# Kernel tuning notes

Measured on AMD Instinct MI355X. Metric: run time of the kernel, lower is better.

## Reference

```python
import jax, jax.numpy as jnp
import numpy as np

NUM_HEADS = 16

def setup_inputs() -> dict:
    key = jax.random.key(0)
    ks = jax.random.split(key, 5)
    b, s, d = 4, 1024, 1024
    scale = 0.02
    return {
        "x": jax.random.normal(ks[0], (b, s, d), dtype=jnp.float32),
        "Wq": jax.random.normal(ks[1], (d, d), dtype=jnp.float32) * scale,
        "Wk": jax.random.normal(ks[2], (d, d), dtype=jnp.float32) * scale,
        "Wv": jax.random.normal(ks[3], (d, d), dtype=jnp.float32) * scale,
        "Wo": jax.random.normal(ks[4], (d, d), dtype=jnp.float32) * scale,
        "bo": jnp.zeros((d,), dtype=jnp.float32),
    }

def reference(x, Wq, Wk, Wv, Wo, bo):
    b, s, d_in = x.shape
    h = NUM_HEADS
    hd = Wq.shape[0] // h  # head_dim
    # torch Linear: y = x @ W.T ; reshape to [b, s, h, hd] then transpose to [b, h, s, hd]
    q = (x @ Wq.T).reshape(b, s, h, hd).transpose(0, 2, 1, 3)
    k = (x @ Wk.T).reshape(b, s, h, hd).transpose(0, 2, 1, 3)
    v = (x @ Wv.T).reshape(b, s, h, hd).transpose(0, 2, 1, 3)
    # attention scores [b, h, s, s]
    scores = jnp.einsum('bhqd,bhkd->bhqk', q, k)
    # NOTE: the original calls masked_fill (NOT masked_fill_), which returns a
    # new tensor that is discarded -> the causal mask is never actually applied.
    # We faithfully reproduce that: no mask.
    attn = jax.nn.softmax(scores / jnp.sqrt(jnp.float32(hd)), axis=-1)
    # dropout p=0.0 -> identity
    ctx = jnp.einsum('bhqk,bhkd->bhqd', attn, v)  # [b, h, s, hd]
    ctx = ctx.transpose(0, 2, 1, 3).reshape(b, s, h * hd)
    return ctx @ Wo.T + bo
```

## Files before the change

kernel.cpp:

```cpp
#include <hip/hip_runtime.h>
#include <hip/hip_bf16.h>

#define BB 4
#define SS 1024
#define DD 1024
#define HH 16
#define HDIM 64
#define MM (BB*SS)

typedef __attribute__((ext_vector_type(8))) short  bf16x8;
typedef __attribute__((ext_vector_type(4))) float  f32x4v;
typedef __attribute__((ext_vector_type(4))) unsigned short u16x4;

static __device__ __forceinline__ unsigned short f2bf(float f) {
    union { float f; unsigned u; } v; v.f = f;
    unsigned r = v.u + 0x7fff + ((v.u >> 16) & 1);
    return (unsigned short)(r >> 16);
}

static __device__ __forceinline__ void gload16(const void* g, const void* lds_uniform_base) {
    __builtin_amdgcn_global_load_lds(
        (const __attribute__((address_space(1))) unsigned int*)(uintptr_t)g,
        (__attribute__((address_space(3))) unsigned int*)(uintptr_t)lds_uniform_base,
        16, 0, 0);
}

__global__ __launch_bounds__(256) void convert_x(
    const float* __restrict__ x, unsigned short* __restrict__ xb)
{
    size_t i = ((size_t)blockIdx.x * 256 + threadIdx.x) * 4;
    f32x4v v = *(const f32x4v*)(x + i);
    u16x4 o;
    o[0] = f2bf(v[0]); o[1] = f2bf(v[1]); o[2] = f2bf(v[2]); o[3] = f2bf(v[3]);
    *(u16x4*)(xb + i) = o;
}

__global__ __launch_bounds__(256) void qkv_gemm(
    const unsigned short* __restrict__ xb,
    const float* __restrict__ Wq, const float* __restrict__ Wk,
    const float* __restrict__ Wv,
    unsigned short* __restrict__ q_ws, unsigned short* __restrict__ k_ws,
    unsigned short* __restrict__ v_ws)
{
    const int bn = blockIdx.x, bm = blockIdx.y, bz = blockIdx.z;
    const float* W = (bz == 0) ? Wq : (bz == 1) ? Wk : Wv;
    unsigned short* outp = (bz == 0) ? q_ws : (bz == 1) ? k_ws : v_ws;

    const int tid = threadIdx.x;
    const int wid = tid >> 6, lane = tid & 63;
    const int wr = wid >> 1, wc = wid & 1;
    const int lhi = lane >> 4, llo = lane & 15;

    __shared__ unsigned short As[2][128 * 32];
    __shared__ unsigned short Bs[2][128 * 32];

    const int m0 = bm * 128, n0 = bn * 128;
    const int brow = tid >> 1, bhalf = tid & 1;

    auto stageA = [&](int buf, int kt) {
        #pragma unroll
        for (int j = 0; j < 2; ++j) {
            int chunk = j * 256 + wid * 64 + lane;
            int row = chunk >> 2, sub = chunk & 3;
            gload16(xb + (size_t)(m0 + row) * DD + kt * 32 + sub * 8,
                    &As[buf][(j * 256 + wid * 64) * 8]);
        }
    };
    auto loadB = [&](int kt, f32x4v* r) {
        const float* p = W + (size_t)(n0 + brow) * DD + kt * 32 + bhalf * 16;
        r[0] = *(const f32x4v*)(p);
        r[1] = *(const f32x4v*)(p + 4);
        r[2] = *(const f32x4v*)(p + 8);
        r[3] = *(const f32x4v*)(p + 12);
    };
    auto writeB = [&](int buf, const f32x4v* r) {
        bf16x8 p0, p1;
        #pragma unroll
        for (int e = 0; e < 4; ++e) {
            p0[e]     = (short)f2bf(r[0][e]);
            p0[e + 4] = (short)f2bf(r[1][e]);
            p1[e]     = (short)f2bf(r[2][e]);
            p1[e + 4] = (short)f2bf(r[3][e]);
        }
        *(bf16x8*)&Bs[buf][brow * 32 + bhalf * 16]     = p0;
        *(bf16x8*)&Bs[buf][brow * 32 + bhalf * 16 + 8] = p1;
    };

    f32x4v acc[4][4] = {};
    f32x4v br[4];

    stageA(0, 0);
    loadB(0, br);
    writeB(0, br);
    __syncthreads();

    for (int kt = 0; kt < 32; ++kt) {
        int cur = kt & 1;
        if (kt < 31) { loadB(kt + 1, br); stageA(cur ^ 1, kt + 1); }

        bf16x8 af[4], bfr[4];
        #pragma unroll
        for (int i = 0; i < 4; ++i)
            af[i] = *(const bf16x8*)&As[cur][(wr * 64 + i * 16 + llo) * 32 + lhi * 8];
        #pragma unroll
        for (int i = 0; i < 4; ++i)
            bfr[i] = *(const bf16x8*)&Bs[cur][(wc * 64 + i * 16 + llo) * 32 + lhi * 8];

        #pragma unroll
        for (int i = 0; i < 4; ++i)
            #pragma unroll
            for (int j = 0; j < 4; ++j)
                acc[i][j] = __builtin_amdgcn_mfma_f32_16x16x32_bf16(af[i], bfr[j], acc[i][j], 0, 0, 0);

        if (kt < 31) writeB(cur ^ 1, br);
        __syncthreads();
    }

    const float sc = (bz == 0) ? 0.125f : 1.0f;
    #pragma unroll
    for (int i = 0; i < 4; ++i) {
        #pragma unroll
        for (int j = 0; j < 4; ++j) {
            #pragma unroll
            for (int r = 0; r < 4; ++r) {
                int mrow = m0 + wr * 64 + i * 16 + lhi * 4 + r;
                int ncol = n0 + wc * 64 + j * 16 + llo;
                float val = acc[i][j][r] * sc;
                size_t idx = ((size_t)((mrow >> 10) * HH + (ncol >> 6)) * SS + (mrow & 1023)) * HDIM + (ncol & 63);
                outp[idx] = f2bf(val);
            }
        }
    }
}

__global__ __launch_bounds__(256) void attn_kernel(
    const unsigned short* __restrict__ q_ws,
    const unsigned short* __restrict__ k_ws,
    const unsigned short* __restrict__ v_ws,
    unsigned short* __restrict__ ctx)
{
    const int qt = blockIdx.x;
    const int bh = blockIdx.y;
    const int tid = threadIdx.x, wid = tid >> 6, lane = tid & 63;
    const int lhi = lane >> 4, llo = lane & 15;

    __shared__ unsigned short Ks[2][64 * 64];
    __shared__ unsigned short Vs[2][64 * 64];
    __shared__ unsigned short Ps[4][16 * 72];

    const size_t basekv = (size_t)bh * SS * HDIM;
    const int qrow0 = qt * 64 + wid * 16;

    bf16x8 aq[2];
    #pragma unroll
    for (int ks = 0; ks < 2; ++ks)
        aq[ks] = *(const bf16x8*)(q_ws + basekv + (size_t)(qrow0 + llo) * HDIM + ks * 32 + lhi * 8);

    auto stage = [&](int buf, int kvt) {
        #pragma unroll
        for (int j = 0; j < 2; ++j) {
            int chunk = j * 256 + wid * 64 + lane;
            int krow = chunk >> 3, ksub = chunk & 7;
            gload16(k_ws + basekv + (size_t)(kvt * 64 + krow) * HDIM + ((ksub ^ (krow & 7)) * 8),
                    &Ks[buf][(j * 256 + wid * 64) * 8]);
            gload16(v_ws + basekv + (size_t)(kvt * 64 + krow) * HDIM + ksub * 8,
                    &Vs[buf][(j * 256 + wid * 64) * 8]);
        }
    };

    f32x4v o[4] = {};
    float m_run[4], l_run[4];
    #pragma unroll
    for (int j = 0; j < 4; ++j) { m_run[j] = -1e30f; l_run[j] = 0.f; }

    stage(0, 0);
    __syncthreads();

    for (int kvt = 0; kvt < 16; ++kvt) {
        const int cur = kvt & 1;
        if (kvt < 15) stage(cur ^ 1, kvt + 1);

        const char* kbuf = (const char*)&Ks[cur][0];
        f32x4v s[4] = {};
        #pragma unroll
        for (int ni = 0; ni < 4; ++ni) {
            int row = ni * 16 + llo;
            #pragma unroll
            for (int ks = 0; ks < 2; ++ks) {
                int colb = (ks * 64 + lhi * 16) ^ ((llo & 7) << 4);
                bf16x8 bk = *(const bf16x8*)(kbuf + row * 128 + colb);
                s[ni] = __builtin_amdgcn_mfma_f32_16x16x32_bf16(aq[ks], bk, s[ni], 0, 0, 0);
            }
        }

        #pragma unroll
        for (int j = 0; j < 4; ++j) {
            float tmax = fmaxf(fmaxf(s[0][j], s[1][j]), fmaxf(s[2][j], s[3][j]));
            #pragma unroll
            for (int off = 1; off < 16; off <<= 1)
                tmax = fmaxf(tmax, __shfl_xor(tmax, off, 64));
            float mn = fmaxf(m_run[j], tmax);
            float alpha = __expf(m_run[j] - mn);
            float rs = 0.f;
            #pragma unroll
            for (int ni = 0; ni < 4; ++ni) {
                float p = __expf(s[ni][j] - mn);
                s[ni][j] = p;
                rs += p;
            }
            #pragma unroll
            for (int off = 1; off < 16; off <<= 1)
                rs += __shfl_xor(rs, off, 64);
            l_run[j] = l_run[j] * alpha + rs;
            m_run[j] = mn;
            #pragma unroll
            for (int ni = 0; ni < 4; ++ni) o[ni][j] *= alpha;
        }

        unsigned short* pw = Ps[wid];
        #pragma unroll
        for (int ni = 0; ni < 4; ++ni)
            #pragma unroll
            for (int j = 0; j < 4; ++j)
                pw[(lhi * 4 + j) * 72 + ni * 16 + llo] = f2bf(s[ni][j]);

        asm volatile("s_waitcnt lgkmcnt(0)" ::: "memory");
        __builtin_amdgcn_sched_barrier(0);

        bf16x8 pa[2];
        #pragma unroll
        for (int ks = 0; ks < 2; ++ks)
            pa[ks] = *(const bf16x8*)(pw + llo * 72 + ks * 32 + lhi * 8);

        const unsigned short* vbuf = &Vs[cur][0];
        #pragma unroll
        for (int ks = 0; ks < 2; ++ks) {
            #pragma unroll
            for (int ni = 0; ni < 4; ++ni) {
                bf16x8 bv;
                #pragma unroll
                for (int e = 0; e < 8; ++e)
                    bv[e] = (short)vbuf[(ks * 32 + lhi * 8 + e) * 64 + ni * 16 + llo];
                o[ni] = __builtin_amdgcn_mfma_f32_16x16x32_bf16(pa[ks], bv, o[ni], 0, 0, 0);
            }
        }
        __syncthreads();
    }

    const int b = bh >> 4, h = bh & 15;
    float rinv[4];
    #pragma unroll
    for (int j = 0; j < 4; ++j) rinv[j] = 1.0f / l_run[j];
    #pragma unroll
    for (int ni = 0; ni < 4; ++ni) {
        #pragma unroll
        for (int j = 0; j < 4; ++j) {
            int srow = qrow0 + lhi * 4 + j;
            int hd = ni * 16 + llo;
            ctx[(size_t)(b * SS + srow) * DD + h * HDIM + hd] = f2bf(o[ni][j] * rinv[j]);
        }
    }
}

__global__ __launch_bounds__(256) void out_gemm(
    const unsigned short* __restrict__ ctx,
    const float* __restrict__ Wo,
    const float* __restrict__ bo,
    float* __restrict__ out)
{
    const int bn = blockIdx.x, bm = blockIdx.y;
    const int tid = threadIdx.x;
    const int wid = tid >> 6, lane = tid & 63;
    const int wr = wid >> 1, wc = wid & 1;
    const int lhi = lane >> 4, llo = lane & 15;

    __shared__ unsigned short As[2][128 * 32];
    __shared__ unsigned short Bs[2][128 * 32];

    const int m0 = bm * 128, n0 = bn * 128;
    const int brow = tid >> 1, bhalf = tid & 1;

    auto stageA = [&](int buf, int kt) {
        #pragma unroll
        for (int j = 0; j < 2; ++j) {
            int chunk = j * 256 + wid * 64 + lane;
            int row = chunk >> 2, sub = chunk & 3;
            gload16(ctx + (size_t)(m0 + row) * DD + kt * 32 + sub * 8,
                    &As[buf][(j * 256 + wid * 64) * 8]);
        }
    };
    auto loadB = [&](int kt, f32x4v* r) {
        const float* p = Wo + (size_t)(n0 + brow) * DD + kt * 32 + bhalf * 16;
        r[0] = *(const f32x4v*)(p);
        r[1] = *(const f32x4v*)(p + 4);
        r[2] = *(const f32x4v*)(p + 8);
        r[3] = *(const f32x4v*)(p + 12);
    };
    auto writeB = [&](int buf, const f32x4v* r) {
        bf16x8 p0, p1;
        #pragma unroll
        for (int e = 0; e < 4; ++e) {
            p0[e]     = (short)f2bf(r[0][e]);
            p0[e + 4] = (short)f2bf(r[1][e]);
            p1[e]     = (short)f2bf(r[2][e]);
            p1[e + 4] = (short)f2bf(r[3][e]);
        }
        *(bf16x8*)&Bs[buf][brow * 32 + bhalf * 16]     = p0;
        *(bf16x8*)&Bs[buf][brow * 32 + bhalf * 16 + 8] = p1;
    };

    f32x4v acc[4][4] = {};
    f32x4v br[4];

    stageA(0, 0);
    loadB(0, br);
    writeB(0, br);
    __syncthreads();

    for (int kt = 0; kt < 32; ++kt) {
        int cur = kt & 1;
        if (kt < 31) { loadB(kt + 1, br); stageA(cur ^ 1, kt + 1); }

        bf16x8 af[4], bfr[4];
        #pragma unroll
        for (int i = 0; i < 4; ++i)
            af[i] = *(const bf16x8*)&As[cur][(wr * 64 + i * 16 + llo) * 32 + lhi * 8];
        #pragma unroll
        for (int i = 0; i < 4; ++i)
            bfr[i] = *(const bf16x8*)&Bs[cur][(wc * 64 + i * 16 + llo) * 32 + lhi * 8];

        #pragma unroll
        for (int i = 0; i < 4; ++i)
            #pragma unroll
            for (int j = 0; j < 4; ++j)
                acc[i][j] = __builtin_amdgcn_mfma_f32_16x16x32_bf16(af[i], bfr[j], acc[i][j], 0, 0, 0);

        if (kt < 31) writeB(cur ^ 1, br);
        __syncthreads();
    }

    #pragma unroll
    for (int j = 0; j < 4; ++j) {
        int ncol = n0 + wc * 64 + j * 16 + llo;
        float bias = bo[ncol];
        #pragma unroll
        for (int i = 0; i < 4; ++i) {
            #pragma unroll
            for (int r = 0; r < 4; ++r) {
                int mrow = m0 + wr * 64 + i * 16 + lhi * 4 + r;
                out[(size_t)mrow * DD + ncol] = acc[i][j][r] + bias;
            }
        }
    }
}

extern "C" void kernel_launch(void* const* d_in, const int* in_sizes, int n_in,
                              void* d_out, int out_size, void* d_ws, size_t ws_size,
                              hipStream_t stream) {
    const float* x  = (const float*)d_in[0];
    const float* Wq = (const float*)d_in[1];
    const float* Wk = (const float*)d_in[2];
    const float* Wv = (const float*)d_in[3];
    const float* Wo = (const float*)d_in[4];
    const float* bo = (const float*)d_in[5];
    float* out = (float*)d_out;

    unsigned short* xb   = (unsigned short*)d_ws;
    unsigned short* q_ws = xb   + (size_t)MM * DD;
    unsigned short* k_ws = q_ws + (size_t)MM * DD;
    unsigned short* v_ws = k_ws + (size_t)MM * DD;
    unsigned short* ctx  = xb;

    convert_x<<<4096, 256, 0, stream>>>(x, xb);
    qkv_gemm<<<dim3(8, 32, 3), 256, 0, stream>>>(xb, Wq, Wk, Wv, q_ws, k_ws, v_ws);
    attn_kernel<<<dim3(16, 64), 256, 0, stream>>>(q_ws, k_ws, v_ws, ctx);
    out_gemm<<<dim3(8, 32), 256, 0, stream>>>(ctx, Wo, bo, out);
}
```

Baseline: 240.7 us.

## Pre-convert weights to bf16 and store V transposed for vectorized attention loads

Adds a kernel that converts all four weight matrices to bf16 once, so the QKV and output GEMMs can stage both operands with direct global-to-LDS loads instead of converting fp32 weights in registers. V is now written transposed (head_dim by seq) with vector stores, and the attention kernel loads it with an XOR swizzle, so each B fragment becomes a single 16-byte LDS read instead of eight scalar strided reads. The new path is used only when the workspace is at least 40 MB, otherwise the old path runs. It adds one launch and extra workspace traffic for the converted weights.

```diff
diff --git a/kernel.cpp b/kernel.cpp
--- a/kernel.cpp
+++ b/kernel.cpp
@@ -35,7 +35,119 @@
     *(u16x4*)(xb + i) = o;
 }
 
-__global__ __launch_bounds__(256) void qkv_gemm(
+__global__ __launch_bounds__(256) void convert_w(
+    const float* __restrict__ Wq, const float* __restrict__ Wk,
+    const float* __restrict__ Wv, const float* __restrict__ Wo,
+    unsigned short* __restrict__ wqb, unsigned short* __restrict__ wkb,
+    unsigned short* __restrict__ wvb, unsigned short* __restrict__ wob)
+{
+    const int seg = blockIdx.y;
+    const float* src = (seg == 0) ? Wq : (seg == 1) ? Wk : (seg == 2) ? Wv : Wo;
+    unsigned short* dst = (seg == 0) ? wqb : (seg == 1) ? wkb : (seg == 2) ? wvb : wob;
+    size_t i = ((size_t)blockIdx.x * 256 + threadIdx.x) * 4;
+    f32x4v v = *(const f32x4v*)(src + i);
+    u16x4 o;
+    o[0] = f2bf(v[0]); o[1] = f2bf(v[1]); o[2] = f2bf(v[2]); o[3] = f2bf(v[3]);
+    *(u16x4*)(dst + i) = o;
+}
+
+static __device__ __forceinline__ void qkv_epilogue(
+    int bz, int m0, int n0, int wr, int wc, int lhi, int llo,
+    const f32x4v acc[4][4], unsigned short* outp)
+{
+    if (bz == 2) {
+        #pragma unroll
+        for (int i = 0; i < 4; ++i) {
+            #pragma unroll
+            for (int j = 0; j < 4; ++j) {
+                int mb = m0 + wr * 64 + i * 16 + lhi * 4;
+                int ncol = n0 + wc * 64 + j * 16 + llo;
+                u16x4 o4;
+                #pragma unroll
+                for (int r = 0; r < 4; ++r) o4[r] = f2bf(acc[i][j][r]);
+                size_t idx = ((size_t)((mb >> 10) * HH + (ncol >> 6)) * HDIM + (ncol & 63)) * SS + (mb & 1023);
+                *(u16x4*)(outp + idx) = o4;
+            }
+        }
+    } else {
+        const float sc = (bz == 0) ? 0.125f : 1.0f;
+        #pragma unroll
+        for (int i = 0; i < 4; ++i) {
+            #pragma unroll
+            for (int j = 0; j < 4; ++j) {
+                #pragma unroll
+                for (int r = 0; r < 4; ++r) {
+                    int mrow = m0 + wr * 64 + i * 16 + lhi * 4 + r;
+                    int ncol = n0 + wc * 64 + j * 16 + llo;
+                    size_t idx = ((size_t)((mrow >> 10) * HH + (ncol >> 6)) * SS + (mrow & 1023)) * HDIM + (ncol & 63);
+                    outp[idx] = f2bf(acc[i][j][r] * sc);
+                }
+            }
+        }
+    }
+}
+
+__global__ __launch_bounds__(256) void qkv_gemm_pc(
+    const unsigned short* __restrict__ xb,
+    const unsigned short* __restrict__ wqb, const unsigned short* __restrict__ wkb,
+    const unsigned short* __restrict__ wvb,
+    unsigned short* __restrict__ q_ws, unsigned short* __restrict__ k_ws,
+    unsigned short* __restrict__ v_ws)
+{
+    const int bn = blockIdx.x, bm = blockIdx.y, bz = blockIdx.z;
+    const unsigned short* W = (bz == 0) ? wqb : (bz == 1) ? wkb : wvb;
+    unsigned short* outp = (bz == 0) ? q_ws : (bz == 1) ? k_ws : v_ws;
+
+    const int tid = threadIdx.x;
+    const int wid = tid >> 6, lane = tid & 63;
+    const int wr = wid >> 1, wc = wid & 1;
+    const int lhi = lane >> 4, llo = lane & 15;
+
+    __shared__ unsigned short As[2][128 * 32];
+    __shared__ unsigned short Bs[2][128 * 32];
+
+    const int m0 = bm * 128, n0 = bn * 128;
+
+    auto stage = [&](int buf, int kt) {
+        #pragma unroll
+        for (int j = 0; j < 2; ++j) {
+            int chunk = j * 256 + wid * 64 + lane;
+            int row = chunk >> 2, sub = chunk & 3;
+            gload16(xb + (size_t)(m0 + row) * DD + kt * 32 + sub * 8,
+                    &As[buf][(j * 256 + wid * 64) * 8]);
+            gload16(W + (size_t)(n0 + row) * DD + kt * 32 + sub * 8,
+                    &Bs[buf][(j * 256 + wid * 64) * 8]);
+        }
+    };
+
+    f32x4v acc[4][4] = {};
+    stage(0, 0);
+    __syncthreads();
+
+    for (int kt = 0; kt < 32; ++kt) {
+        int cur = kt & 1;
+        if (kt < 31) stage(cur ^ 1, kt + 1);
+
+        bf16x8 af[4], bfr[4];
+        #pragma unroll
+        for (int i = 0; i < 4; ++i)
+            af[i] = *(const bf16x8*)&As[cur][(wr * 64 + i * 16 + llo) * 32 + lhi * 8];
+        #pragma unroll
+        for (int i = 0; i < 4; ++i)
+            bfr[i] = *(const bf16x8*)&Bs[cur][(wc * 64 + i * 16 + llo) * 32 + lhi * 8];
+
+        #pragma unroll
+        for (int i = 0; i < 4; ++i)
+            #pragma unroll
+            for (int j = 0; j < 4; ++j)
+                acc[i][j] = __builtin_amdgcn_mfma_f32_16x16x32_bf16(af[i], bfr[j], acc[i][j], 0, 0, 0);
+        __syncthreads();
+    }
+
+    qkv_epilogue(bz, m0, n0, wr, wc, lhi, llo, acc, outp);
+}
+
+__global__ __launch_bounds__(256) void qkv_gemm_rs(
     const unsigned short* __restrict__ xb,
     const float* __restrict__ Wq, const float* __restrict__ Wk,
     const float* __restrict__ Wv,
@@ -116,27 +228,13 @@
         __syncthreads();
     }
 
-    const float sc = (bz == 0) ? 0.125f : 1.0f;
-    #pragma unroll
-    for (int i = 0; i < 4; ++i) {
-        #pragma unroll
-        for (int j = 0; j < 4; ++j) {
-            #pragma unroll
-            for (int r = 0; r < 4; ++r) {
-                int mrow = m0 + wr * 64 + i * 16 + lhi * 4 + r;
-                int ncol = n0 + wc * 64 + j * 16 + llo;
-                float val = acc[i][j][r] * sc;
-                size_t idx = ((size_t)((mrow >> 10) * HH + (ncol >> 6)) * SS + (mrow & 1023)) * HDIM + (ncol & 63);
-                outp[idx] = f2bf(val);
-            }
-        }
-    }
+    qkv_epilogue(bz, m0, n0, wr, wc, lhi, llo, acc, outp);
 }
 
 __global__ __launch_bounds__(256) void attn_kernel(
     const unsigned short* __restrict__ q_ws,
     const unsigned short* __restrict__ k_ws,
-    const unsigned short* __restrict__ v_ws,
+    const unsigned short* __restrict__ vt_ws,
     unsigned short* __restrict__ ctx)
 {
     const int qt = blockIdx.x;
@@ -160,10 +258,11 @@
         #pragma unroll
         for (int j = 0; j < 2; ++j) {
             int chunk = j * 256 + wid * 64 + lane;
-            int krow = chunk >> 3, ksub = chunk & 7;
-            gload16(k_ws + basekv + (size_t)(kvt * 64 + krow) * HDIM + ((ksub ^ (krow & 7)) * 8),
+            int row = chunk >> 3, sub = chunk & 7;
+            int ssub = (sub ^ (row & 7)) * 8;
+            gload16(k_ws + basekv + (size_t)(kvt * 64 + row) * HDIM + ssub,
                     &Ks[buf][(j * 256 + wid * 64) * 8]);
-            gload16(v_ws + basekv + (size_t)(kvt * 64 + krow) * HDIM + ksub * 8,
+            gload16(vt_ws + basekv + (size_t)row * SS + kvt * 64 + ssub,
                     &Vs[buf][(j * 256 + wid * 64) * 8]);
         }
     };
@@ -232,15 +331,13 @@
         for (int ks = 0; ks < 2; ++ks)
             pa[ks] = *(const bf16x8*)(pw + llo * 72 + ks * 32 + lhi * 8);
 
-        const unsigned short* vbuf = &Vs[cur][0];
+        const char* vbuf = (const char*)&Vs[cur][0];
         #pragma unroll
         for (int ks = 0; ks < 2; ++ks) {
             #pragma unroll
             for (int ni = 0; ni < 4; ++ni) {
-                bf16x8 bv;
-                #pragma unroll
-                for (int e = 0; e < 8; ++e)
-                    bv[e] = (short)vbuf[(ks * 32 + lhi * 8 + e) * 64 + ni * 16 + llo];
+                int colb = (ks * 64 + lhi * 16) ^ ((llo & 7) << 4);
+                bf16x8 bv = *(const bf16x8*)(vbuf + (ni * 16 + llo) * 128 + colb);
                 o[ni] = __builtin_amdgcn_mfma_f32_16x16x32_bf16(pa[ks], bv, o[ni], 0, 0, 0);
             }
         }
@@ -262,7 +359,75 @@
     }
 }
 
-__global__ __launch_bounds__(256) void out_gemm(
+__global__ __launch_bounds__(256) void out_gemm_pc(
+    const unsigned short* __restrict__ ctx,
+    const unsigned short* __restrict__ wob,
+    const float* __restrict__ bo,
+    float* __restrict__ out)
+{
+    const int bn = blockIdx.x, bm = blockIdx.y;
+    const int tid = threadIdx.x;
+    const int wid = tid >> 6, lane = tid & 63;
+    const int wr = wid >> 1, wc = wid & 1;
+    const int lhi = lane >> 4, llo = lane & 15;
+
+    __shared__ unsigned short As[2][128 * 32];
+    __shared__ unsigned short Bs[2][128 * 32];
+
+    const int m0 = bm * 128, n0 = bn * 128;
+
+    auto stage = [&](int buf, int kt) {
+        #pragma unroll
+        for (int j = 0; j < 2; ++j) {
+            int chunk = j * 256 + wid * 64 + lane;
+            int row = chunk >> 2, sub = chunk & 3;
+            gload16(ctx + (size_t)(m0 + row) * DD + kt * 32 + sub * 8,
+                    &As[buf][(j * 256 + wid * 64) * 8]);
+            gload16(wob + (size_t)(n0 + row) * DD + kt * 32 + sub * 8,
+                    &Bs[buf][(j * 256 + wid * 64) * 8]);
+        }
+    };
+
+    f32x4v acc[4][4] = {};
+    stage(0, 0);
+    __syncthreads();
+
+    for (int kt = 0; kt < 32; ++kt) {
+        int cur = kt & 1;
+        if (kt < 31) stage(cur ^ 1, kt + 1);
+
+        bf16x8 af[4], bfr[4];
+        #pragma unroll
+        for (int i = 0; i < 4; ++i)
+            af[i] = *(const bf16x8*)&As[cur][(wr * 64 + i * 16 + llo) * 32 + lhi * 8];
+        #pragma unroll
+        for (int i = 0; i < 4; ++i)
+            bfr[i] = *(const bf16x8*)&Bs[cur][(wc * 64 + i * 16 + llo) * 32 + lhi * 8];
+
+        #pragma unroll
+        for (int i = 0; i < 4; ++i)
+            #pragma unroll
+            for (int j = 0; j < 4; ++j)
+                acc[i][j] = __builtin_amdgcn_mfma_f32_16x16x32_bf16(af[i], bfr[j], acc[i][j], 0, 0, 0);
+        __syncthreads();
+    }
+
+    #pragma unroll
+    for (int j = 0; j < 4; ++j) {
+        int ncol = n0 + wc * 64 + j * 16 + llo;
+        float bias = bo[ncol];
+        #pragma unroll
+        for (int i = 0; i < 4; ++i) {
+            #pragma unroll
+            for (int r = 0; r < 4; ++r) {
+                int mrow = m0 + wr * 64 + i * 16 + lhi * 4 + r;
+                out[(size_t)mrow * DD + ncol] = acc[i][j][r] + bias;
+            }
+        }
+    }
+}
+
+__global__ __launch_bounds__(256) void out_gemm_rs(
     const unsigned short* __restrict__ ctx,
     const float* __restrict__ Wo,
     const float* __restrict__ bo,
@@ -365,14 +530,34 @@
     const float* bo = (const float*)d_in[5];
     float* out = (float*)d_out;
 
-    unsigned short* xb   = (unsigned short*)d_ws;
-    unsigned short* q_ws = xb   + (size_t)MM * DD;
-    unsigned short* k_ws = q_ws + (size_t)MM * DD;
-    unsigned short* v_ws = k_ws + (size_t)MM * DD;
-    unsigned short* ctx  = xb;
-
-    convert_x<<<4096, 256, 0, stream>>>(x, xb);
-    qkv_gemm<<<dim3(8, 32, 3), 256, 0, stream>>>(xb, Wq, Wk, Wv, q_ws, k_ws, v_ws);
-    attn_kernel<<<dim3(16, 64), 256, 0, stream>>>(q_ws, k_ws, v_ws, ctx);
-    out_gemm<<<dim3(8, 32), 256, 0, stream>>>(ctx, Wo, bo, out);
-}
+    const bool preconv = ws_size >= (size_t)40 * 1024 * 1024;
+
+    if (preconv) {
+        unsigned short* xb   = (unsigned short*)d_ws;
+        unsigned short* wqb  = xb   + (size_t)MM * DD;
+        unsigned short* wkb  = wqb  + (size_t)DD * DD;
+        unsigned short* wvb  = wkb  + (size_t)DD * DD;
+        unsigned short* wob  = wvb  + (size_t)DD * DD;
+        unsigned short* q_ws = wob  + (size_t)DD * DD;
+        unsigned short* k_ws = q_ws + (size_t)MM * DD;
+        unsigned short* v_ws = k_ws + (size_t)MM * DD;
+        unsigned short* ctx  = xb;
+
+        convert_x<<<4096, 256, 0, stream>>>(x, xb);
+        convert_w<<<dim3(1024, 4), 256, 0, stream>>>(Wq, Wk, Wv, Wo, wqb, wkb, wvb, wob);
+        qkv_gemm_pc<<<dim3(8, 32, 3), 256, 0, stream>>>(xb, wqb, wkb, wvb, q_ws, k_ws, v_ws);
+        attn_kernel<<<dim3(16, 64), 256, 0, stream>>>(q_ws, k_ws, v_ws, ctx);
+        out_gemm_pc<<<dim3(8, 32), 256, 0, stream>>>(ctx, wob, bo, out);
+    } else {
+        unsigned short* xb   = (unsigned short*)d_ws;
+        unsigned short* q_ws = xb   + (size_t)MM * DD;
+        unsigned short* k_ws = q_ws + (size_t)MM * DD;
+        unsigned short* v_ws = k_ws + (size_t)MM * DD;
+        unsigned short* ctx  = xb;
+
+        convert_x<<<4096, 256, 0, stream>>>(x, xb);
+        qkv_gemm_rs<<<dim3(8, 32, 3), 256, 0, stream>>>(xb, Wq, Wk, Wv, q_ws, k_ws, v_ws);
+        attn_kernel<<<dim3(16, 64), 256, 0, stream>>>(q_ws, k_ws, v_ws, ctx);
+        out_gemm_rs<<<dim3(8, 32), 256, 0, stream>>>(ctx, Wo, bo, out);
+    }
+}
```

New measurement: 202.2 us. -16.0%, faster.
